# Performance work log

Measured on AMD Instinct MI355X. Metric: run time of the kernel, lower is better.

Reference implementation:

```python
import jax, jax.numpy as jnp
import numpy as np

BIT = 8
QMAX = 2 ** (BIT - 1) - 1   # 127
QMIN = -(2 ** (BIT - 1))    # -128


def _quant_linear(x, W, b, act_sf):
    """HAWQ-style QuantLinear: per-output-channel symmetric 8-bit weights,
    integer GEMM on the (already-quantized) activation grid, dequantized output.
    Returns (out, weight_scaling_factor)."""
    w_sf = jnp.max(jnp.abs(W), axis=1) / QMAX                      # [out]
    w_int = jnp.clip(jnp.round(W / w_sf[:, None]), QMIN, QMAX)     # [out,in]
    x_int = x / act_sf                                             # integer-valued floats
    b_int = jnp.round(b / (w_sf * act_sf))                         # [out]
    out = (jnp.einsum('bsd,od->bso', x_int, w_int) + b_int) * (w_sf * act_sf)
    return out, w_sf


def _quant_act(x):
    """QuantAct: per-tensor symmetric 8-bit requantization."""
    sf = jnp.max(jnp.abs(x)) / QMAX
    xq = jnp.clip(jnp.round(x / sf), QMIN, QMAX) * sf
    return xq, sf


def setup_inputs() -> dict:
    key = jax.random.key(0)
    k = jax.random.split(key, 5)
    B, S, D, H = 256, 196, 384, 1536
    act_scaling_factor = jnp.array([0.05], jnp.float32)
    x = jax.random.normal(k[0], (B, S, D), jnp.float32)
    # input arrives already fake-quantized on the act_scaling_factor grid
    x = jnp.clip(jnp.round(x / act_scaling_factor), QMIN, QMAX) * act_scaling_factor
    W1 = jax.random.normal(k[1], (H, D), jnp.float32) * 0.02
    b1 = jax.random.normal(k[2], (H,), jnp.float32) * 0.02
    W2 = jax.random.normal(k[3], (D, H), jnp.float32) * 0.02
    b2 = jax.random.normal(k[4], (D,), jnp.float32) * 0.02
    return dict(x=x, W1=W1, b1=b1, W2=W2, b2=b2,
                act_scaling_factor=act_scaling_factor)


def reference(x, W1, b1, W2, b2, act_scaling_factor):
    h, _ = _quant_linear(x, W1, b1, act_scaling_factor)
    h = jax.nn.relu(h)
    h, asf1 = _quant_act(h)
    y, _ = _quant_linear(h, W2, b2, asf1)
    y, asf2 = _quant_act(y)
    return y, asf2
```

## Files before the change

### kernel.cpp

```cpp
#include <hip/hip_runtime.h>
#include <hip/hip_bf16.h>
#include <stdint.h>


#define M_TOT 50176
#define D_IN  384
#define H_MID 1536
#define OUT_N (M_TOT * D_IN)
#define NSLOT 256

typedef int v4i __attribute__((ext_vector_type(4)));

__device__ __forceinline__ float clamp_q(float q) {
  return fminf(fmaxf(q, -128.0f), 127.0f);
}

__device__ __forceinline__ float fast_div(float t, float d, float R) {
  const float q1 = t * R;
  const float r  = fmaf(-d, q1, t);
  return fmaf(r, R, q1);
}

__device__ __forceinline__ void gld_lds16(const int8_t* g, int8_t* s) {
  __builtin_amdgcn_global_load_lds((const __attribute__((address_space(1))) void*)g,
                                   (__attribute__((address_space(3))) void*)s,
                                   16, 0, 0);
}


__global__ void quant_w_kernel(const float* __restrict__ W, const float* __restrict__ b,
                               int8_t* __restrict__ Wq, float* __restrict__ wsf,
                               int* __restrict__ bint, const float* __restrict__ asf_p,
                               int cols) {
  const int lane = threadIdx.x & 63;
  const int row  = blockIdx.x * 4 + (threadIdx.x >> 6);
  const float* wr = W + (size_t)row * cols;
  float m = 0.f;
  for (int c = lane; c < cols; c += 64) m = fmaxf(m, fabsf(wr[c]));
#pragma unroll
  for (int off = 32; off; off >>= 1) m = fmaxf(m, __shfl_xor(m, off));
  const float sf = m / 127.0f;
  int8_t* qbase = Wq + (size_t)(row >> 4) * 16 * cols + (row & 15) * 16;
  for (int c = lane; c < cols; c += 64)
    qbase[(c >> 4) * 256 + (c & 15)] = (int8_t)clamp_q(rintf(wr[c] / sf));
  if (lane == 0) {
    wsf[row] = sf;
    if (bint) bint[row] = (int)rintf(b[row] / (sf * asf_p[0]));
  }
}

__global__ void quant_x_kernel(const float* __restrict__ x, int8_t* __restrict__ xq,
                               const float* __restrict__ asf_p) {
  const int lane = threadIdx.x & 63;
  const int wid  = threadIdx.x >> 6;
  const float R = 1.0f / asf_p[0];
  const int r  = lane & 15;
  const int kq = lane >> 4;
  const int ntask = (M_TOT / 16) * 6;
  for (int task = blockIdx.x * 4 + wid; task < ntask; task += gridDim.x * 4) {
    const int pan = task / 6;
    const int kcq = task - pan * 6;
    const float* src = x + ((size_t)pan * 16 + r) * D_IN + (kcq * 4 + kq) * 16;
    int out[4];
#pragma unroll
    for (int q4 = 0; q4 < 4; ++q4) {
      float4 v = *(const float4*)(src + q4 * 4);
      unsigned a0 = (unsigned char)(signed char)clamp_q(rintf(v.x * R));
      unsigned a1 = (unsigned char)(signed char)clamp_q(rintf(v.y * R));
      unsigned a2 = (unsigned char)(signed char)clamp_q(rintf(v.z * R));
      unsigned a3 = (unsigned char)(signed char)clamp_q(rintf(v.w * R));
      out[q4] = (int)(a0 | (a1 << 8) | (a2 << 16) | (a3 << 24));
    }
    *(int4*)(xq + (size_t)pan * 6144 + kcq * 1024 + lane * 16) = *(int4*)out;
  }
}

template <int MODE>
__global__ __launch_bounds__(256, 4) void gemm_i8_kernel(
    const int8_t* __restrict__ A, const int8_t* __restrict__ Bm,
    int K, int nchunks, int ntiles_n,
    const float* __restrict__ sfv, const int* __restrict__ bintv,
    const float* __restrict__ bias, const float* __restrict__ asf_p,
    const unsigned* __restrict__ gmax_in,
    float* __restrict__ Cout, int8_t* __restrict__ Cq,
    unsigned* __restrict__ gmax_out) {
  __shared__ __align__(16) int8_t sA[24576];
  __shared__ __align__(16) int8_t sB[12288];
  __shared__ float bcastv[4];
  const int tid    = threadIdx.x;
  const int lane   = tid & 63;
  const int wid    = tid >> 6;
  const int tid16  = tid * 16;
  const int lane16 = lane * 16;
  const int cpx = gridDim.x >> 3;
  const int wg  = (blockIdx.x & 7) * cpx + (blockIdx.x >> 3);
  const int bn = wg % ntiles_n;
  const int bm = wg / ntiles_n;
  const int l16 = lane & 15;

  if (MODE != 0 && wid == 0) {
    float m = fmaxf(fmaxf(__uint_as_float(gmax_in[lane]),
                          __uint_as_float(gmax_in[lane + 64])),
                    fmaxf(__uint_as_float(gmax_in[lane + 128]),
                          __uint_as_float(gmax_in[lane + 192])));
#pragma unroll
    for (int off = 32; off; off >>= 1) m = fmaxf(m, __shfl_xor(m, off));
    if (lane == 0) bcastv[0] = m / 127.0f;
  }

  const int8_t* gA0 = A  + (size_t)(bm * 128) * K;
  const int8_t* gB0 = Bm + (size_t)(bn * 64) * K;
  int aoff[6], boff[3];
#pragma unroll
  for (int l = 0; l < 6; ++l) {
    const int s = l * 256 + tid;
    const int rb = s / 192, rem = s - rb * 192;
    aoff[l] = rb * 16 * K + (rem >> 4) * 256 + (rem & 15) * 16;
  }
#pragma unroll
  for (int l = 0; l < 3; ++l) {
    const int s = l * 256 + tid;
    const int rb = s / 192, rem = s - rb * 192;
    boff[l] = rb * 16 * K + (rem >> 4) * 256 + (rem & 15) * 16;
  }

  const int wmblk = (wid >> 1) * 4;
  const int wnblk = (wid & 1) * 2;

  v4i acc[4][2] = {};

  for (int c = 0; c < nchunks; ++c) {
    const int cb = c * 3072;
#pragma unroll
    for (int l = 0; l < 6; ++l) gld_lds16(gA0 + aoff[l] + cb, sA + l * 4096 + tid16);
#pragma unroll
    for (int l = 0; l < 3; ++l) gld_lds16(gB0 + boff[l] + cb, sB + l * 4096 + tid16);
    __syncthreads();
#pragma unroll
    for (int ks = 0; ks < 3; ++ks) {
      v4i va[4], vb[2];
#pragma unroll
      for (int i = 0; i < 4; ++i)
        va[i] = *(const v4i*)&sA[(wmblk + i) * 3072 + ks * 1024 + lane16];
#pragma unroll
      for (int j = 0; j < 2; ++j)
        vb[j] = *(const v4i*)&sB[(wnblk + j) * 3072 + ks * 1024 + lane16];
#pragma unroll
      for (int i = 0; i < 4; ++i)
#pragma unroll
        for (int j = 0; j < 2; ++j)
          acc[i][j] = __builtin_amdgcn_mfma_i32_16x16x64_i8(va[i], vb[j], acc[i][j], 0, 0, 0);
    }
    __syncthreads();
  }

  const int wm = (wid >> 1) * 64;
  const int wn = (wid & 1) * 32;
  const int r0 = (lane >> 4) * 4;
  float lmax = 0.f;

  if (MODE == 0) {
#pragma unroll
    for (int j = 0; j < 2; ++j) {
      int mi = acc[0][j][0];
#pragma unroll
      for (int i = 0; i < 4; ++i)
#pragma unroll
        for (int r = 0; r < 4; ++r) mi = max(mi, acc[i][j][r]);
      const int col = bn * 64 + wn + j * 16 + l16;
      lmax = fmaxf(lmax, (float)(mi + bintv[col]) * (sfv[col] * asf_p[0]));
    }
  } else if (MODE == 1) {
    const float sf1 = bcastv[0];
    const float R   = 1.0f / sf1;
    const float asf = asf_p[0];
#pragma unroll
    for (int j = 0; j < 2; ++j) {
      const int col = bn * 64 + wn + j * 16 + l16;
      const float scale = sfv[col] * asf;
      const int bi = bintv[col];
      const size_t cc = (size_t)((bn * 4 + (wid & 1) * 2 + j) << 8);
#pragma unroll
      for (int i = 0; i < 4; ++i) {
        const size_t prow = (size_t)(bm * 8 + (wid >> 1) * 4 + i) * (16 * H_MID);
#pragma unroll
        for (int r = 0; r < 4; ++r) {
          const float t = fmaxf((float)(acc[i][j][r] + bi) * scale, 0.f);
          const float q = fminf(rintf(fast_div(t, sf1, R)), 127.0f);
          Cq[prow + cc + (size_t)((r0 + r) * 16 + l16)] = (int8_t)q;
        }
      }
    }
  } else {
    const float sf1 = bcastv[0];
#pragma unroll
    for (int j = 0; j < 2; ++j) {
      const int col = bn * 64 + wn + j * 16 + l16;
      const float scale = sfv[col] * sf1;
      const int bi = (int)rintf(bias[col] / scale);
      int mi = acc[0][j][0], mn = acc[0][j][0];
#pragma unroll
      for (int i = 0; i < 4; ++i) {
        const int row = bm * 128 + wm + i * 16 + r0;
#pragma unroll
        for (int r = 0; r < 4; ++r) {
          const int a = acc[i][j][r];
          mi = max(mi, a); mn = min(mn, a);
          Cout[(size_t)(row + r) * D_IN + col] = (float)(a + bi) * scale;
        }
      }
      lmax = fmaxf(lmax, fmaxf(fabsf((float)(mi + bi) * scale),
                               fabsf((float)(mn + bi) * scale)));
    }
  }

  if (MODE != 1) {
#pragma unroll
    for (int off = 32; off; off >>= 1) lmax = fmaxf(lmax, __shfl_xor(lmax, off));
    if (lane == 0) atomicMax(&gmax_out[(wg * 4 + wid) & (NSLOT - 1)], __float_as_uint(lmax));
  }
}

__global__ void final_quant_kernel(float* __restrict__ y, const unsigned* __restrict__ slots,
                                   int n4) {
  __shared__ float s_sf;
  const int tid = threadIdx.x;
  if (tid < 64) {
    float m = fmaxf(fmaxf(__uint_as_float(slots[tid]),
                          __uint_as_float(slots[tid + 64])),
                    fmaxf(__uint_as_float(slots[tid + 128]),
                          __uint_as_float(slots[tid + 192])));
#pragma unroll
    for (int off = 32; off; off >>= 1) m = fmaxf(m, __shfl_xor(m, off));
    if (tid == 0) s_sf = m / 127.0f;
  }
  __syncthreads();
  const float asf2 = s_sf;
  const float R = 1.0f / asf2;
  float4* y4 = (float4*)y;
  const int stride = gridDim.x * blockDim.x;
  for (int i = blockIdx.x * blockDim.x + tid; i < n4; i += stride) {
    float4 v = y4[i];
    v.x = clamp_q(rintf(fast_div(v.x, asf2, R))) * asf2;
    v.y = clamp_q(rintf(fast_div(v.y, asf2, R))) * asf2;
    v.z = clamp_q(rintf(fast_div(v.z, asf2, R))) * asf2;
    v.w = clamp_q(rintf(fast_div(v.w, asf2, R))) * asf2;
    y4[i] = v;
  }
  if (blockIdx.x == 0 && tid == 0) y[(size_t)n4 * 4] = asf2;
}

extern "C" void kernel_launch(void* const* d_in, const int* in_sizes, int n_in,
                              void* d_out, int out_size, void* d_ws, size_t ws_size,
                              hipStream_t stream) {
  const float* x   = (const float*)d_in[0];
  const float* W1  = (const float*)d_in[1];
  const float* b1  = (const float*)d_in[2];
  const float* W2  = (const float*)d_in[3];
  const float* b2  = (const float*)d_in[4];
  const float* asf = (const float*)d_in[5];

  char* ws = (char*)d_ws;
  unsigned* gmax1 = (unsigned*)ws;
  unsigned* gmax2 = (unsigned*)(ws + 1024);
  size_t off = 4096;
  int8_t* xq   = (int8_t*)(ws + off); off += (size_t)M_TOT * D_IN;
  int8_t* w1q  = (int8_t*)(ws + off); off += (size_t)H_MID * D_IN;
  float*  w1sf = (float*)(ws + off);  off += (size_t)H_MID * 4;
  int*    b1i  = (int*)(ws + off);    off += (size_t)H_MID * 4;
  int8_t* w2q  = (int8_t*)(ws + off); off += (size_t)D_IN * H_MID;
  float*  w2sf = (float*)(ws + off);  off += (size_t)D_IN * 4;
  off = (off + 255) & ~(size_t)255;
  int8_t* hq   = (int8_t*)(ws + off); off += (size_t)M_TOT * H_MID;

  hipMemsetAsync(d_ws, 0, 4096, stream);

  quant_w_kernel<<<H_MID / 4, 256, 0, stream>>>(W1, b1, w1q, w1sf, b1i, asf, D_IN);
  quant_w_kernel<<<D_IN / 4, 256, 0, stream>>>(W2, nullptr, w2q, w2sf, nullptr, nullptr, H_MID);
  quant_x_kernel<<<2048, 256, 0, stream>>>(x, xq, asf);

  const int g1 = (M_TOT / 128) * (H_MID / 64);
  const int g2 = (M_TOT / 128) * (D_IN / 64);
  gemm_i8_kernel<0><<<g1, 256, 0, stream>>>(
      xq, w1q, D_IN, 2, H_MID / 64, w1sf, b1i, nullptr, asf,
      nullptr, nullptr, nullptr, gmax1);
  gemm_i8_kernel<1><<<g1, 256, 0, stream>>>(
      xq, w1q, D_IN, 2, H_MID / 64, w1sf, b1i, nullptr, asf,
      gmax1, nullptr, hq, nullptr);
  gemm_i8_kernel<2><<<g2, 256, 0, stream>>>(
      hq, w2q, H_MID, 8, D_IN / 64, w2sf, nullptr, b2, nullptr,
      gmax1, (float*)d_out, nullptr, gmax2);
  final_quant_kernel<<<2048, 256, 0, stream>>>((float*)d_out, gmax2, OUT_N / 4);
}
```

Measured before the change: 215.3 us.

## Load GEMM operands directly from global into registers, dropping LDS staging

Replaces the LDS-staged GEMM main loop (global_load_lds into shared memory plus barriers) with per-wave direct global loads of pre-packed 16x64 fragments into registers. A double-buffered register prefetch overlaps the next k-step's loads with the current MFMAs. This removes shared-memory traffic and __syncthreads. The cost is that operand tiles shared between waves are now fetched separately by each wave through the cache rather than once per block. The MODE 1 epilogue is also simplified to one multiply by a precomputed ratio instead of scale followed by a refined division, which can change rounding at ties relative to the previous division path.

```diff
diff --git a/kernel.cpp b/kernel.cpp
--- a/kernel.cpp
+++ b/kernel.cpp
@@ -19,12 +19,6 @@
   const float q1 = t * R;
   const float r  = fmaf(-d, q1, t);
   return fmaf(r, R, q1);
-}
-
-__device__ __forceinline__ void gld_lds16(const int8_t* g, int8_t* s) {
-  __builtin_amdgcn_global_load_lds((const __attribute__((address_space(1))) void*)g,
-                                   (__attribute__((address_space(3))) void*)s,
-                                   16, 0, 0);
 }
 
 
@@ -78,80 +72,68 @@
 template <int MODE>
 __global__ __launch_bounds__(256, 4) void gemm_i8_kernel(
     const int8_t* __restrict__ A, const int8_t* __restrict__ Bm,
-    int K, int nchunks, int ntiles_n,
+    int K, int ntiles_n,
     const float* __restrict__ sfv, const int* __restrict__ bintv,
     const float* __restrict__ bias, const float* __restrict__ asf_p,
     const unsigned* __restrict__ gmax_in,
     float* __restrict__ Cout, int8_t* __restrict__ Cq,
     unsigned* __restrict__ gmax_out) {
-  __shared__ __align__(16) int8_t sA[24576];
-  __shared__ __align__(16) int8_t sB[12288];
-  __shared__ float bcastv[4];
-  const int tid    = threadIdx.x;
-  const int lane   = tid & 63;
-  const int wid    = tid >> 6;
-  const int tid16  = tid * 16;
-  const int lane16 = lane * 16;
+  const int tid  = threadIdx.x;
+  const int lane = tid & 63;
+  const int wid  = tid >> 6;
   const int cpx = gridDim.x >> 3;
   const int wg  = (blockIdx.x & 7) * cpx + (blockIdx.x >> 3);
   const int bn = wg % ntiles_n;
   const int bm = wg / ntiles_n;
   const int l16 = lane & 15;
 
-  if (MODE != 0 && wid == 0) {
+  const int rbA = bm * 8 + (wid >> 1) * 4;
+  const int rbB = bn * 4 + (wid & 1) * 2;
+  const int sK  = 16 * K;
+  const int8_t* pa = A  + (size_t)rbA * sK + lane * 16;
+  const int8_t* pb = Bm + (size_t)rbB * sK + lane * 16;
+
+  v4i acc[4][2] = {};
+  const int ksteps = K >> 6;
+
+  v4i a0[4], b0[2], a1[4], b1[2];
+#pragma unroll
+  for (int i = 0; i < 4; ++i) a0[i] = *(const v4i*)(pa + i * sK);
+#pragma unroll
+  for (int j = 0; j < 2; ++j) b0[j] = *(const v4i*)(pb + j * sK);
+
+  for (int ks = 0; ks < ksteps; ks += 2) {
+#pragma unroll
+    for (int i = 0; i < 4; ++i) a1[i] = *(const v4i*)(pa + i * sK + (ks + 1) * 1024);
+#pragma unroll
+    for (int j = 0; j < 2; ++j) b1[j] = *(const v4i*)(pb + j * sK + (ks + 1) * 1024);
+#pragma unroll
+    for (int i = 0; i < 4; ++i)
+#pragma unroll
+      for (int j = 0; j < 2; ++j)
+        acc[i][j] = __builtin_amdgcn_mfma_i32_16x16x64_i8(a0[i], b0[j], acc[i][j], 0, 0, 0);
+    if (ks + 2 < ksteps) {
+#pragma unroll
+      for (int i = 0; i < 4; ++i) a0[i] = *(const v4i*)(pa + i * sK + (ks + 2) * 1024);
+#pragma unroll
+      for (int j = 0; j < 2; ++j) b0[j] = *(const v4i*)(pb + j * sK + (ks + 2) * 1024);
+    }
+#pragma unroll
+    for (int i = 0; i < 4; ++i)
+#pragma unroll
+      for (int j = 0; j < 2; ++j)
+        acc[i][j] = __builtin_amdgcn_mfma_i32_16x16x64_i8(a1[i], b1[j], acc[i][j], 0, 0, 0);
+  }
+
+  float sf1 = 0.f;
+  if (MODE != 0) {
     float m = fmaxf(fmaxf(__uint_as_float(gmax_in[lane]),
                           __uint_as_float(gmax_in[lane + 64])),
                     fmaxf(__uint_as_float(gmax_in[lane + 128]),
                           __uint_as_float(gmax_in[lane + 192])));
 #pragma unroll
     for (int off = 32; off; off >>= 1) m = fmaxf(m, __shfl_xor(m, off));
-    if (lane == 0) bcastv[0] = m / 127.0f;
-  }
-
-  const int8_t* gA0 = A  + (size_t)(bm * 128) * K;
-  const int8_t* gB0 = Bm + (size_t)(bn * 64) * K;
-  int aoff[6], boff[3];
-#pragma unroll
-  for (int l = 0; l < 6; ++l) {
-    const int s = l * 256 + tid;
-    const int rb = s / 192, rem = s - rb * 192;
-    aoff[l] = rb * 16 * K + (rem >> 4) * 256 + (rem & 15) * 16;
-  }
-#pragma unroll
-  for (int l = 0; l < 3; ++l) {
-    const int s = l * 256 + tid;
-    const int rb = s / 192, rem = s - rb * 192;
-    boff[l] = rb * 16 * K + (rem >> 4) * 256 + (rem & 15) * 16;
-  }
-
-  const int wmblk = (wid >> 1) * 4;
-  const int wnblk = (wid & 1) * 2;
-
-  v4i acc[4][2] = {};
-
-  for (int c = 0; c < nchunks; ++c) {
-    const int cb = c * 3072;
-#pragma unroll
-    for (int l = 0; l < 6; ++l) gld_lds16(gA0 + aoff[l] + cb, sA + l * 4096 + tid16);
-#pragma unroll
-    for (int l = 0; l < 3; ++l) gld_lds16(gB0 + boff[l] + cb, sB + l * 4096 + tid16);
-    __syncthreads();
-#pragma unroll
-    for (int ks = 0; ks < 3; ++ks) {
-      v4i va[4], vb[2];
-#pragma unroll
-      for (int i = 0; i < 4; ++i)
-        va[i] = *(const v4i*)&sA[(wmblk + i) * 3072 + ks * 1024 + lane16];
-#pragma unroll
-      for (int j = 0; j < 2; ++j)
-        vb[j] = *(const v4i*)&sB[(wnblk + j) * 3072 + ks * 1024 + lane16];
-#pragma unroll
-      for (int i = 0; i < 4; ++i)
-#pragma unroll
-        for (int j = 0; j < 2; ++j)
-          acc[i][j] = __builtin_amdgcn_mfma_i32_16x16x64_i8(va[i], vb[j], acc[i][j], 0, 0, 0);
-    }
-    __syncthreads();
+    sf1 = m / 127.0f;
   }
 
   const int wm = (wid >> 1) * 64;
@@ -171,13 +153,11 @@
       lmax = fmaxf(lmax, (float)(mi + bintv[col]) * (sfv[col] * asf_p[0]));
     }
   } else if (MODE == 1) {
-    const float sf1 = bcastv[0];
-    const float R   = 1.0f / sf1;
     const float asf = asf_p[0];
 #pragma unroll
     for (int j = 0; j < 2; ++j) {
       const int col = bn * 64 + wn + j * 16 + l16;
-      const float scale = sfv[col] * asf;
+      const float ratio = (sfv[col] * asf) / sf1;
       const int bi = bintv[col];
       const size_t cc = (size_t)((bn * 4 + (wid & 1) * 2 + j) << 8);
 #pragma unroll
@@ -185,14 +165,13 @@
         const size_t prow = (size_t)(bm * 8 + (wid >> 1) * 4 + i) * (16 * H_MID);
 #pragma unroll
         for (int r = 0; r < 4; ++r) {
-          const float t = fmaxf((float)(acc[i][j][r] + bi) * scale, 0.f);
-          const float q = fminf(rintf(fast_div(t, sf1, R)), 127.0f);
+          const float f = (float)(acc[i][j][r] + bi);
+          const float q = fminf(fmaxf(rintf(f * ratio), 0.f), 127.0f);
           Cq[prow + cc + (size_t)((r0 + r) * 16 + l16)] = (int8_t)q;
         }
       }
     }
   } else {
-    const float sf1 = bcastv[0];
 #pragma unroll
     for (int j = 0; j < 2; ++j) {
       const int col = bn * 64 + wn + j * 16 + l16;
@@ -282,13 +261,13 @@
   const int g1 = (M_TOT / 128) * (H_MID / 64);
   const int g2 = (M_TOT / 128) * (D_IN / 64);
   gemm_i8_kernel<0><<<g1, 256, 0, stream>>>(
-      xq, w1q, D_IN, 2, H_MID / 64, w1sf, b1i, nullptr, asf,
+      xq, w1q, D_IN, H_MID / 64, w1sf, b1i, nullptr, asf,
       nullptr, nullptr, nullptr, gmax1);
   gemm_i8_kernel<1><<<g1, 256, 0, stream>>>(
-      xq, w1q, D_IN, 2, H_MID / 64, w1sf, b1i, nullptr, asf,
+      xq, w1q, D_IN, H_MID / 64, w1sf, b1i, nullptr, asf,
       gmax1, nullptr, hq, nullptr);
   gemm_i8_kernel<2><<<g2, 256, 0, stream>>>(
-      hq, w2q, H_MID, 8, D_IN / 64, w2sf, nullptr, b2, nullptr,
+      hq, w2q, H_MID, D_IN / 64, w2sf, nullptr, b2, nullptr,
       gmax1, (float*)d_out, nullptr, gmax2);
   final_quant_kernel<<<2048, 256, 0, stream>>>((float*)d_out, gmax2, OUT_N / 4);
 }
```

New measurement: 233.1 us. +8.3%, slower.
